# Kernel optimization log

Measured on AMD Instinct MI355X. Metric: run time of the kernel, lower is better.

## Reference

```python
import jax, jax.numpy as jnp
import numpy as np

B, S, D, H = 2, 2048, 768, 12
DK = D // H

def setup_inputs() -> dict:
    key = jax.random.key(0)
    ks = jax.random.split(key, 11)
    sc = 0.02
    inp = {
        'Q': jax.random.normal(ks[0], (B, S, D), jnp.float32),
        'K': jax.random.normal(ks[1], (B, S, D), jnp.float32),
        'V': jax.random.normal(ks[2], (B, S, D), jnp.float32),
        # causal mask, broadcastable over batch and heads (1 = keep, 0 = mask)
        'mask': jnp.tril(jnp.ones((S, S), jnp.int32))[None, None, :, :],
        'Wq': jax.random.normal(ks[3], (D, D), jnp.float32) * sc,
        'bq': jax.random.normal(ks[4], (D,), jnp.float32) * sc,
        'Wk': jax.random.normal(ks[5], (D, D), jnp.float32) * sc,
        'bk': jax.random.normal(ks[6], (D,), jnp.float32) * sc,
        'Wv': jax.random.normal(ks[7], (D, D), jnp.float32) * sc,
        'bv': jax.random.normal(ks[8], (D,), jnp.float32) * sc,
        'Wo': jax.random.normal(ks[9], (D, D), jnp.float32) * sc,
        'bo': jax.random.normal(ks[10], (D,), jnp.float32) * sc,
    }
    return inp

def _split_heads(x):
    # [B,S,D] -> [B,H,S,DK]
    return x.reshape(B, S, H, DK).transpose(0, 2, 1, 3)

def reference(Q, K, V, mask, Wq, bq, Wk, bk, Wv, bv, Wo, bo):
    # torch Linear: y = x @ W.T + b
    q = _split_heads(Q @ Wq.T + bq)
    k = _split_heads(K @ Wk.T + bk)
    v = _split_heads(V @ Wv.T + bv)
    scores = jnp.einsum('bhqd,bhkd->bhqk', q, k) / jnp.sqrt(jnp.float32(DK))
    scores = jnp.where(mask == 0, jnp.float32(-1e9), scores)
    attn = jax.nn.softmax(scores, axis=-1)
    out = jnp.einsum('bhqk,bhkd->bhqd', attn, v)  # [B,H,S,DK]
    out = out.transpose(0, 2, 1, 3).reshape(B, S, D)
    return out @ Wo.T + bo
```

## Files before the change

kernel.cpp:

```cpp
#include <hip/hip_runtime.h>
#include <hip/hip_bf16.h>

#define H_  12
#define S_  2048
#define D_  768
#define DK_ 64

typedef __bf16 bf16x8 __attribute__((ext_vector_type(8)));
typedef __bf16 bf16x4 __attribute__((ext_vector_type(4)));
typedef short  short4v __attribute__((ext_vector_type(4)));
typedef float  f32x4  __attribute__((ext_vector_type(4)));

__device__ inline f32x4 mfma_bf16(bf16x8 a, bf16x8 b, f32x4 c) {
  return __builtin_amdgcn_mfma_f32_16x16x32_bf16(a, b, c, 0, 0, 0);
}

__device__ inline f32x4 mfma16(bf16x4 a, bf16x4 b, f32x4 c) {
#if __has_builtin(__builtin_amdgcn_mfma_f32_16x16x16bf16_1k)
  short4v as = __builtin_bit_cast(short4v, a);
  short4v bs = __builtin_bit_cast(short4v, b);
  return __builtin_amdgcn_mfma_f32_16x16x16bf16_1k(as, bs, c, 0, 0, 0);
#else
  asm("s_nop 1\n\tv_mfma_f32_16x16x16_bf16 %0, %1, %2, %0"
      : "+v"(c) : "v"(a), "v"(b));
  return c;
#endif
}

__device__ inline bf16x8 cvt2bf16(f32x4 a, f32x4 b) {
  bf16x8 r;
  r[0] = (__bf16)a[0]; r[1] = (__bf16)a[1];
  r[2] = (__bf16)a[2]; r[3] = (__bf16)a[3];
  r[4] = (__bf16)b[0]; r[5] = (__bf16)b[1];
  r[6] = (__bf16)b[2]; r[7] = (__bf16)b[3];
  return r;
}

__global__ __launch_bounds__(256, 4)
void qkv_proj(const float* __restrict__ Q, const float* __restrict__ K,
              const float* __restrict__ V,
              const float* __restrict__ Wq, const float* __restrict__ Wk,
              const float* __restrict__ Wv,
              const float* __restrict__ bq, const float* __restrict__ bk,
              const float* __restrict__ bv,
              __hip_bfloat16* __restrict__ q_ws,
              __hip_bfloat16* __restrict__ k_ws,
              __hip_bfloat16* __restrict__ vT_ws)
{
  __shared__ alignas(16) __hip_bfloat16 Ald[2][64][40];
  __shared__ alignas(16) __hip_bfloat16 Bld[2][128][40];

  const int z = blockIdx.z;
  const float* X    = (z == 0) ? Q  : (z == 1) ? K  : V;
  const float* W    = (z == 0) ? Wq : (z == 1) ? Wk : Wv;
  const float* bias = (z == 0) ? bq : (z == 1) ? bk : bv;
  __hip_bfloat16* out = (z == 0) ? q_ws : (z == 1) ? k_ws : vT_ws;
  const bool vmode = (z == 2);
  const float osc = (z == 0) ? 0.125f : 1.0f;

  const int t    = threadIdx.x;
  const int w    = t >> 6;
  const int lane = t & 63;
  const int l15  = lane & 15;
  const int quad = lane >> 4;
  const int m0 = blockIdx.x * 64;
  const int n0 = blockIdx.y * 128;
  const int wm = (w >> 1) * 32;
  const int wn = (w & 1) * 64;

  const f32x4 fzero = {0.f, 0.f, 0.f, 0.f};
  f32x4 acc[2][4];
#pragma unroll
  for (int i = 0; i < 2; ++i)
#pragma unroll
    for (int j = 0; j < 4; ++j) acc[i][j] = fzero;

  const int arow = t >> 2, agr = t & 3;
  const float* Asrc  = X + (size_t)(m0 + arow) * D_ + agr * 8;
  const float* Bsrc0 = W + (size_t)(n0 + arow) * D_ + agr * 8;
  const float* Bsrc1 = W + (size_t)(n0 + arow + 64) * D_ + agr * 8;

  f32x4 a0 = *(const f32x4*)(Asrc), a1 = *(const f32x4*)(Asrc + 4);
  f32x4 b00 = *(const f32x4*)(Bsrc0), b01 = *(const f32x4*)(Bsrc0 + 4);
  f32x4 b10 = *(const f32x4*)(Bsrc1), b11 = *(const f32x4*)(Bsrc1 + 4);
  *(bf16x8*)&Ald[0][arow][agr * 8]      = cvt2bf16(a0, a1);
  *(bf16x8*)&Bld[0][arow][agr * 8]      = cvt2bf16(b00, b01);
  *(bf16x8*)&Bld[0][arow + 64][agr * 8] = cvt2bf16(b10, b11);

  for (int k0 = 0; k0 < D_; k0 += 32) {
    const int p = (k0 >> 5) & 1;
    __syncthreads();
    const int kn = k0 + 32;
    if (kn < D_) {
      a0  = *(const f32x4*)(Asrc + kn);  a1  = *(const f32x4*)(Asrc + kn + 4);
      b00 = *(const f32x4*)(Bsrc0 + kn); b01 = *(const f32x4*)(Bsrc0 + kn + 4);
      b10 = *(const f32x4*)(Bsrc1 + kn); b11 = *(const f32x4*)(Bsrc1 + kn + 4);
    }

    bf16x8 af[2], bfr[4];
#pragma unroll
    for (int i = 0; i < 2; ++i) af[i]  = *(const bf16x8*)&Ald[p][wm + 16 * i + l15][quad * 8];
#pragma unroll
    for (int j = 0; j < 4; ++j) bfr[j] = *(const bf16x8*)&Bld[p][wn + 16 * j + l15][quad * 8];
#pragma unroll
    for (int i = 0; i < 2; ++i)
#pragma unroll
      for (int j = 0; j < 4; ++j)
        acc[i][j] = mfma_bf16(af[i], bfr[j], acc[i][j]);

    if (kn < D_) {
      *(bf16x8*)&Ald[p ^ 1][arow][agr * 8]      = cvt2bf16(a0, a1);
      *(bf16x8*)&Bld[p ^ 1][arow][agr * 8]      = cvt2bf16(b00, b01);
      *(bf16x8*)&Bld[p ^ 1][arow + 64][agr * 8] = cvt2bf16(b10, b11);
    }
  }

#pragma unroll
  for (int j = 0; j < 4; ++j) {
    const int n_g = n0 + wn + 16 * j + l15;
    const float bv = bias[n_g];
    const int hh = n_g >> 6, dk = n_g & (DK_ - 1);
#pragma unroll
    for (int i = 0; i < 2; ++i) {
      const int mbase = m0 + wm + 16 * i + quad * 4;
#pragma unroll
      for (int r = 0; r < 4; ++r) {
        const int m_g = mbase + r;
        const int bb = m_g >> 11, ss = m_g & (S_ - 1);
        const float vout = (acc[i][j][r] + bv) * osc;
        size_t idx;
        if (vmode)
          idx = (((size_t)(bb * H_ + hh)) * DK_ + dk) * S_ + ss;
        else
          idx = (((size_t)(bb * H_ + hh)) * S_ + ss) * DK_ + dk;
        out[idx] = __float2bfloat16(vout);
      }
    }
  }
}

__global__ __launch_bounds__(256, 4)
void o_proj(const __hip_bfloat16* __restrict__ Xb,
            const float* __restrict__ W,
            const float* __restrict__ bias,
            float* __restrict__ outf)
{
  __shared__ alignas(16) __hip_bfloat16 Ald[2][64][40];
  __shared__ alignas(16) __hip_bfloat16 Bld[2][64][40];

  const int t    = threadIdx.x;
  const int w    = t >> 6;
  const int lane = t & 63;
  const int l15  = lane & 15;
  const int quad = lane >> 4;
  const int m0 = blockIdx.x * 64;
  const int n0 = blockIdx.y * 64;
  const int wm = 16 * w;

  const f32x4 fzero = {0.f, 0.f, 0.f, 0.f};
  f32x4 acc[4];
#pragma unroll
  for (int j = 0; j < 4; ++j) acc[j] = fzero;

  const int arow = t >> 2, agr = t & 3;
  const __hip_bfloat16* Asrc = Xb + (size_t)(m0 + arow) * D_ + agr * 8;
  const float* Bsrc = W + (size_t)(n0 + arow) * D_ + agr * 8;

  bf16x8 a_r = *(const bf16x8*)(Asrc);
  f32x4 b0 = *(const f32x4*)(Bsrc), b1 = *(const f32x4*)(Bsrc + 4);
  *(bf16x8*)&Ald[0][arow][agr * 8] = a_r;
  *(bf16x8*)&Bld[0][arow][agr * 8] = cvt2bf16(b0, b1);

  for (int k0 = 0; k0 < D_; k0 += 32) {
    const int p = (k0 >> 5) & 1;
    __syncthreads();
    const int kn = k0 + 32;
    if (kn < D_) {
      a_r = *(const bf16x8*)(Asrc + kn);
      b0 = *(const f32x4*)(Bsrc + kn); b1 = *(const f32x4*)(Bsrc + kn + 4);
    }

    bf16x8 af = *(const bf16x8*)&Ald[p][wm + l15][quad * 8];
    bf16x8 bfr[4];
#pragma unroll
    for (int j = 0; j < 4; ++j) bfr[j] = *(const bf16x8*)&Bld[p][16 * j + l15][quad * 8];
#pragma unroll
    for (int j = 0; j < 4; ++j)
      acc[j] = mfma_bf16(af, bfr[j], acc[j]);

    if (kn < D_) {
      *(bf16x8*)&Ald[p ^ 1][arow][agr * 8] = a_r;
      *(bf16x8*)&Bld[p ^ 1][arow][agr * 8] = cvt2bf16(b0, b1);
    }
  }

#pragma unroll
  for (int j = 0; j < 4; ++j) {
    const int n_g = n0 + 16 * j + l15;
    const float bv = bias[n_g];
    const int mbase = m0 + wm + quad * 4;
#pragma unroll
    for (int r = 0; r < 4; ++r)
      outf[(size_t)(mbase + r) * D_ + n_g] = acc[j][r] + bv;
  }
}

__global__ __launch_bounds__(256, 4)
void flash_attn(const __hip_bfloat16* __restrict__ q_ws,
                const __hip_bfloat16* __restrict__ k_ws,
                const __hip_bfloat16* __restrict__ vT_ws,
                __hip_bfloat16* __restrict__ o_ws)
{
  __shared__ alignas(16) __hip_bfloat16 Kld[128][72];
  __shared__ alignas(16) __hip_bfloat16 Vld[64][136];

  const int t = threadIdx.x, w = t >> 6, lane = t & 63;
  const int l15 = lane & 15, quad = lane >> 4;
  const int bh = blockIdx.y;
  const int b = bh / H_, h = bh % H_;
  const int x = blockIdx.x;
  const int tLo = x, tHi = 63 - x;
  const int myTile = (w < 2) ? tLo : tHi;
  const int qbase = myTile * 32 + 16 * (w & 1);
  const int qg = qbase + l15;
  const int myNkt = (myTile >> 2) + 1;
  const int nktT  = (tHi >> 2) + 1;
  const size_t hbase = (size_t)bh * S_ * DK_;
  const size_t vtb   = (size_t)bh * DK_ * S_;

  bf16x8 qf[2];
#pragma unroll
  for (int kk = 0; kk < 2; ++kk)
    qf[kk] = *(const bf16x8*)(q_ws + hbase + (size_t)qg * DK_ + kk * 32 + quad * 8);

  const f32x4 fzero = {0.f, 0.f, 0.f, 0.f};
  f32x4 accO[4];
#pragma unroll
  for (int jd = 0; jd < 4; ++jd) accO[jd] = fzero;
  float mI = -1.0e30f, lI = 0.f;

  const int tr = t >> 3, kg = t & 7;
  const int tv = t >> 4, vg = t & 15;
  const __hip_bfloat16* Kbase = k_ws + hbase + (size_t)tr * DK_ + kg * 8;
  const __hip_bfloat16* Vbase = vT_ws + vtb + (size_t)tv * S_ + vg * 8;

  bf16x8 rK[4], rV[4];
#pragma unroll
  for (int it = 0; it < 4; ++it) {
    rK[it] = *(const bf16x8*)(Kbase + (size_t)(32 * it) * DK_);
    rV[it] = *(const bf16x8*)(Vbase + (size_t)(16 * it) * S_);
  }

  for (int kt = 0; kt < nktT; ++kt) {
#pragma unroll
    for (int it = 0; it < 4; ++it) {
      *(bf16x8*)&Kld[32 * it + tr][kg * 8] = rK[it];
      *(bf16x8*)&Vld[16 * it + tv][vg * 8] = rV[it];
    }
    __syncthreads();

    if (kt + 1 < nktT) {
      const int k0n = (kt + 1) * 128;
#pragma unroll
      for (int it = 0; it < 4; ++it) {
        rK[it] = *(const bf16x8*)(Kbase + (size_t)(k0n + 32 * it) * DK_);
        rV[it] = *(const bf16x8*)(Vbase + (size_t)(16 * it) * S_ + k0n);
      }
    }

    if (kt < myNkt) {
      const int k0 = kt * 128;
      f32x4 st[8];
#pragma unroll
      for (int j = 0; j < 8; ++j) {
        bf16x8 kf0 = *(const bf16x8*)&Kld[16 * j + l15][quad * 8];
        bf16x8 kf1 = *(const bf16x8*)&Kld[16 * j + l15][32 + quad * 8];
        st[j] = mfma_bf16(kf0, qf[0], fzero);
        st[j] = mfma_bf16(kf1, qf[1], st[j]);
      }

      if (kt == myNkt - 1) {
#pragma unroll
        for (int j = 0; j < 8; ++j)
#pragma unroll
          for (int r = 0; r < 4; ++r) {
            const int kcg = k0 + 16 * j + quad * 4 + r;
            if (kcg > qg) st[j][r] = -1.0e9f;
          }
      }

      float tm = st[0][0];
#pragma unroll
      for (int j = 0; j < 8; ++j)
#pragma unroll
        for (int r = 0; r < 4; ++r) tm = fmaxf(tm, st[j][r]);
      tm = fmaxf(tm, __shfl_xor(tm, 16));
      tm = fmaxf(tm, __shfl_xor(tm, 32));

      const float mnew = fmaxf(mI, tm);
      const float al = __expf(mI - mnew);
      mI = mnew;
      float rs = 0.f;
#pragma unroll
      for (int j = 0; j < 8; ++j)
#pragma unroll
        for (int r = 0; r < 4; ++r) {
          const float pv = __expf(st[j][r] - mnew);
          st[j][r] = pv;
          rs += pv;
        }
      rs += __shfl_xor(rs, 16);
      rs += __shfl_xor(rs, 32);
      lI = lI * al + rs;
#pragma unroll
      for (int jd = 0; jd < 4; ++jd)
#pragma unroll
        for (int r = 0; r < 4; ++r) accO[jd][r] *= al;

      bf16x4 pb[8];
#pragma unroll
      for (int j = 0; j < 8; ++j) {
        pb[j][0] = (__bf16)st[j][0]; pb[j][1] = (__bf16)st[j][1];
        pb[j][2] = (__bf16)st[j][2]; pb[j][3] = (__bf16)st[j][3];
      }

#pragma unroll
      for (int jd = 0; jd < 4; ++jd)
#pragma unroll
        for (int j = 0; j < 8; ++j) {
          bf16x4 vf = *(const bf16x4*)&Vld[16 * jd + l15][16 * j + quad * 4];
          accO[jd] = mfma16(vf, pb[j], accO[jd]);
        }
    }
    __syncthreads();
  }

  const float inv = 1.f / lI;
#pragma unroll
  for (int jd = 0; jd < 4; ++jd) {
    bf16x4 ov;
#pragma unroll
    for (int r = 0; r < 4; ++r) ov[r] = (__bf16)(accO[jd][r] * inv);
    *(bf16x4*)(o_ws + ((size_t)b * S_ + qg) * D_ + h * DK_ + 16 * jd + quad * 4) = ov;
  }
}

extern "C" void kernel_launch(void* const* d_in, const int* in_sizes, int n_in,
                              void* d_out, int out_size, void* d_ws, size_t ws_size,
                              hipStream_t stream) {
  (void)in_sizes; (void)n_in; (void)out_size; (void)ws_size;
  const float* Q  = (const float*)d_in[0];
  const float* K  = (const float*)d_in[1];
  const float* V  = (const float*)d_in[2];
  const float* Wq = (const float*)d_in[4];
  const float* bq = (const float*)d_in[5];
  const float* Wk = (const float*)d_in[6];
  const float* bk = (const float*)d_in[7];
  const float* Wv = (const float*)d_in[8];
  const float* bv = (const float*)d_in[9];
  const float* Wo = (const float*)d_in[10];
  const float* bo = (const float*)d_in[11];
  float* out = (float*)d_out;

  const size_t NEL = (size_t)2 * S_ * D_;
  __hip_bfloat16* q_ws  = (__hip_bfloat16*)d_ws;
  __hip_bfloat16* k_ws  = q_ws  + NEL;
  __hip_bfloat16* vT_ws = k_ws  + NEL;
  __hip_bfloat16* o_ws  = vT_ws + NEL;

  qkv_proj<<<dim3(64, 6, 3), 256, 0, stream>>>(Q, K, V, Wq, Wk, Wv, bq, bk, bv,
                                               q_ws, k_ws, vT_ws);
  flash_attn<<<dim3(32, 24), 256, 0, stream>>>(q_ws, k_ws, vT_ws, o_ws);
  o_proj<<<dim3(64, 12), 256, 0, stream>>>(o_ws, Wo, bo, out);
}
```

Before: 214.1 us.

## Pre-convert weights to bf16, use direct-to-LDS loads, swizzle, larger tiles, exp2 softmax

Adds a kernel that converts all four weight matrices to bf16 once per call. The projection GEMMs then stream the bf16 weights into swizzled, unpadded LDS through global_load_lds, and the tiles grow to 128x128 for QKV and 64x128 for the output projection. The Q scale now includes log2(e), so the attention softmax can use the hardware exp2 instruction. In exchange, double-buffering in LDS is replaced by a single buffer with two barriers per k-step, and the extra conversion kernel adds a launch plus weight traffic.

```diff
diff --git a/kernel.cpp b/kernel.cpp
--- a/kernel.cpp
+++ b/kernel.cpp
@@ -10,6 +10,12 @@
 typedef __bf16 bf16x4 __attribute__((ext_vector_type(4)));
 typedef short  short4v __attribute__((ext_vector_type(4)));
 typedef float  f32x4  __attribute__((ext_vector_type(4)));
+
+#define QSCALE 0.1803368801111137f
+
+__device__ inline float exp2_fast(float x) {
+  return __builtin_amdgcn_exp2f(x);
+}
 
 __device__ inline f32x4 mfma_bf16(bf16x8 a, bf16x8 b, f32x4 c) {
   return __builtin_amdgcn_mfma_f32_16x16x32_bf16(a, b, c, 0, 0, 0);
@@ -27,6 +33,12 @@
 #endif
 }
 
+__device__ inline void gload16(const void* g, void* l) {
+  __builtin_amdgcn_global_load_lds(
+      (const __attribute__((address_space(1))) void*)g,
+      (__attribute__((address_space(3))) void*)l, 16, 0, 0);
+}
+
 __device__ inline bf16x8 cvt2bf16(f32x4 a, f32x4 b) {
   bf16x8 r;
   r[0] = (__bf16)a[0]; r[1] = (__bf16)a[1];
@@ -36,83 +48,107 @@
   return r;
 }
 
-__global__ __launch_bounds__(256, 4)
+__global__ __launch_bounds__(256)
+void conv_w(const float* __restrict__ Wq, const float* __restrict__ Wk,
+            const float* __restrict__ Wv, const float* __restrict__ Wo,
+            __hip_bfloat16* __restrict__ out)
+{
+  const int i8 = blockIdx.x * 256 + threadIdx.x;
+  const int mat = i8 / 73728;
+  const int off = (i8 - mat * 73728) * 8;
+  const float* src = (mat == 0) ? Wq : (mat == 1) ? Wk : (mat == 2) ? Wv : Wo;
+  f32x4 a = *(const f32x4*)(src + off);
+  f32x4 b = *(const f32x4*)(src + off + 4);
+  *(bf16x8*)(out + (size_t)mat * 589824 + off) = cvt2bf16(a, b);
+}
+
+__global__ __launch_bounds__(256, 3)
 void qkv_proj(const float* __restrict__ Q, const float* __restrict__ K,
               const float* __restrict__ V,
-              const float* __restrict__ Wq, const float* __restrict__ Wk,
-              const float* __restrict__ Wv,
+              const __hip_bfloat16* __restrict__ Wb,
               const float* __restrict__ bq, const float* __restrict__ bk,
               const float* __restrict__ bv,
               __hip_bfloat16* __restrict__ q_ws,
               __hip_bfloat16* __restrict__ k_ws,
               __hip_bfloat16* __restrict__ vT_ws)
 {
-  __shared__ alignas(16) __hip_bfloat16 Ald[2][64][40];
-  __shared__ alignas(16) __hip_bfloat16 Bld[2][128][40];
+  __shared__ alignas(16) __hip_bfloat16 Ald[128 * 32];
+  __shared__ alignas(16) __hip_bfloat16 Bld[128 * 32];
 
   const int z = blockIdx.z;
   const float* X    = (z == 0) ? Q  : (z == 1) ? K  : V;
-  const float* W    = (z == 0) ? Wq : (z == 1) ? Wk : Wv;
   const float* bias = (z == 0) ? bq : (z == 1) ? bk : bv;
+  const __hip_bfloat16* Wz = Wb + (size_t)z * 589824;
   __hip_bfloat16* out = (z == 0) ? q_ws : (z == 1) ? k_ws : vT_ws;
   const bool vmode = (z == 2);
-  const float osc = (z == 0) ? 0.125f : 1.0f;
+  const float osc = (z == 0) ? QSCALE : 1.0f;
 
   const int t    = threadIdx.x;
   const int w    = t >> 6;
   const int lane = t & 63;
   const int l15  = lane & 15;
   const int quad = lane >> 4;
-  const int m0 = blockIdx.x * 64;
+  const int m0 = blockIdx.x * 128;
   const int n0 = blockIdx.y * 128;
-  const int wm = (w >> 1) * 32;
+  const int wm = (w >> 1) * 64;
   const int wn = (w & 1) * 64;
 
   const f32x4 fzero = {0.f, 0.f, 0.f, 0.f};
-  f32x4 acc[2][4];
-#pragma unroll
-  for (int i = 0; i < 2; ++i)
+  f32x4 acc[4][4];
+#pragma unroll
+  for (int i = 0; i < 4; ++i)
 #pragma unroll
     for (int j = 0; j < 4; ++j) acc[i][j] = fzero;
 
-  const int arow = t >> 2, agr = t & 3;
-  const float* Asrc  = X + (size_t)(m0 + arow) * D_ + agr * 8;
-  const float* Bsrc0 = W + (size_t)(n0 + arow) * D_ + agr * 8;
-  const float* Bsrc1 = W + (size_t)(n0 + arow + 64) * D_ + agr * 8;
-
-  f32x4 a0 = *(const f32x4*)(Asrc), a1 = *(const f32x4*)(Asrc + 4);
-  f32x4 b00 = *(const f32x4*)(Bsrc0), b01 = *(const f32x4*)(Bsrc0 + 4);
-  f32x4 b10 = *(const f32x4*)(Bsrc1), b11 = *(const f32x4*)(Bsrc1 + 4);
-  *(bf16x8*)&Ald[0][arow][agr * 8]      = cvt2bf16(a0, a1);
-  *(bf16x8*)&Bld[0][arow][agr * 8]      = cvt2bf16(b00, b01);
-  *(bf16x8*)&Bld[0][arow + 64][agr * 8] = cvt2bf16(b10, b11);
+  const int ar = t >> 2, ac = t & 3;
+  const int sw = ac ^ ((ar >> 1) & 3);
+  const float* As0 = X + (size_t)(m0 + ar) * D_ + ac * 8;
+  const float* As1 = X + (size_t)(m0 + ar + 64) * D_ + ac * 8;
+  __hip_bfloat16* Aw0 = &Ald[((ar)      * 4 + sw) * 8];
+  __hip_bfloat16* Aw1 = &Ald[((ar + 64) * 4 + sw) * 8];
+
+  const int bp = (t & 3) ^ (((t >> 2) >> 1) & 3);
+  const __hip_bfloat16* Bs0 = Wz + (size_t)(n0 + (t >> 2)) * D_ + bp * 8;
+  const __hip_bfloat16* Bs1 = Wz + (size_t)(n0 + (t >> 2) + 64) * D_ + bp * 8;
+  __hip_bfloat16* Bd0 = &Bld[t * 8];
+  __hip_bfloat16* Bd1 = &Bld[(t + 256) * 8];
+
+  int agrn[4], bgrn[4];
+#pragma unroll
+  for (int i = 0; i < 4; ++i) {
+    int row = wm + 16 * i + l15;
+    agrn[i] = (row * 4 + (quad ^ ((row >> 1) & 3))) * 8;
+    row = wn + 16 * i + l15;
+    bgrn[i] = (row * 4 + (quad ^ ((row >> 1) & 3))) * 8;
+  }
+
+  f32x4 a00 = *(const f32x4*)As0, a01 = *(const f32x4*)(As0 + 4);
+  f32x4 a10 = *(const f32x4*)As1, a11 = *(const f32x4*)(As1 + 4);
 
   for (int k0 = 0; k0 < D_; k0 += 32) {
-    const int p = (k0 >> 5) & 1;
-    __syncthreads();
+    *(bf16x8*)Aw0 = cvt2bf16(a00, a01);
+    *(bf16x8*)Aw1 = cvt2bf16(a10, a11);
+    gload16(Bs0 + k0, Bd0);
+    gload16(Bs1 + k0, Bd1);
+    __syncthreads();
+
     const int kn = k0 + 32;
     if (kn < D_) {
-      a0  = *(const f32x4*)(Asrc + kn);  a1  = *(const f32x4*)(Asrc + kn + 4);
-      b00 = *(const f32x4*)(Bsrc0 + kn); b01 = *(const f32x4*)(Bsrc0 + kn + 4);
-      b10 = *(const f32x4*)(Bsrc1 + kn); b11 = *(const f32x4*)(Bsrc1 + kn + 4);
-    }
-
-    bf16x8 af[2], bfr[4];
-#pragma unroll
-    for (int i = 0; i < 2; ++i) af[i]  = *(const bf16x8*)&Ald[p][wm + 16 * i + l15][quad * 8];
-#pragma unroll
-    for (int j = 0; j < 4; ++j) bfr[j] = *(const bf16x8*)&Bld[p][wn + 16 * j + l15][quad * 8];
-#pragma unroll
-    for (int i = 0; i < 2; ++i)
+      a00 = *(const f32x4*)(As0 + kn); a01 = *(const f32x4*)(As0 + kn + 4);
+      a10 = *(const f32x4*)(As1 + kn); a11 = *(const f32x4*)(As1 + kn + 4);
+    }
+
+    bf16x8 af[4], bfr[4];
+#pragma unroll
+    for (int i = 0; i < 4; ++i) af[i]  = *(const bf16x8*)&Ald[agrn[i]];
+#pragma unroll
+    for (int j = 0; j < 4; ++j) bfr[j] = *(const bf16x8*)&Bld[bgrn[j]];
+#pragma unroll
+    for (int i = 0; i < 4; ++i)
 #pragma unroll
       for (int j = 0; j < 4; ++j)
         acc[i][j] = mfma_bf16(af[i], bfr[j], acc[i][j]);
-
-    if (kn < D_) {
-      *(bf16x8*)&Ald[p ^ 1][arow][agr * 8]      = cvt2bf16(a0, a1);
-      *(bf16x8*)&Bld[p ^ 1][arow][agr * 8]      = cvt2bf16(b00, b01);
-      *(bf16x8*)&Bld[p ^ 1][arow + 64][agr * 8] = cvt2bf16(b10, b11);
-    }
+    __syncthreads();
   }
 
 #pragma unroll
@@ -121,7 +157,7 @@
     const float bv = bias[n_g];
     const int hh = n_g >> 6, dk = n_g & (DK_ - 1);
 #pragma unroll
-    for (int i = 0; i < 2; ++i) {
+    for (int i = 0; i < 4; ++i) {
       const int mbase = m0 + wm + 16 * i + quad * 4;
 #pragma unroll
       for (int r = 0; r < 4; ++r) {
@@ -141,12 +177,12 @@
 
 __global__ __launch_bounds__(256, 4)
 void o_proj(const __hip_bfloat16* __restrict__ Xb,
-            const float* __restrict__ W,
+            const __hip_bfloat16* __restrict__ Wob,
             const float* __restrict__ bias,
             float* __restrict__ outf)
 {
-  __shared__ alignas(16) __hip_bfloat16 Ald[2][64][40];
-  __shared__ alignas(16) __hip_bfloat16 Bld[2][64][40];
+  __shared__ alignas(16) __hip_bfloat16 Ald[64 * 32];
+  __shared__ alignas(16) __hip_bfloat16 Bld[128 * 32];
 
   const int t    = threadIdx.x;
   const int w    = t >> 6;
@@ -154,54 +190,67 @@
   const int l15  = lane & 15;
   const int quad = lane >> 4;
   const int m0 = blockIdx.x * 64;
-  const int n0 = blockIdx.y * 64;
-  const int wm = 16 * w;
+  const int n0 = blockIdx.y * 128;
+  const int wm = (w >> 1) * 32;
+  const int wn = (w & 1) * 64;
 
   const f32x4 fzero = {0.f, 0.f, 0.f, 0.f};
-  f32x4 acc[4];
-#pragma unroll
-  for (int j = 0; j < 4; ++j) acc[j] = fzero;
-
-  const int arow = t >> 2, agr = t & 3;
-  const __hip_bfloat16* Asrc = Xb + (size_t)(m0 + arow) * D_ + agr * 8;
-  const float* Bsrc = W + (size_t)(n0 + arow) * D_ + agr * 8;
-
-  bf16x8 a_r = *(const bf16x8*)(Asrc);
-  f32x4 b0 = *(const f32x4*)(Bsrc), b1 = *(const f32x4*)(Bsrc + 4);
-  *(bf16x8*)&Ald[0][arow][agr * 8] = a_r;
-  *(bf16x8*)&Bld[0][arow][agr * 8] = cvt2bf16(b0, b1);
+  f32x4 acc[2][4];
+#pragma unroll
+  for (int i = 0; i < 2; ++i)
+#pragma unroll
+    for (int j = 0; j < 4; ++j) acc[i][j] = fzero;
+
+  const int ap = (t & 3) ^ (((t >> 2) >> 1) & 3);
+  const __hip_bfloat16* As  = Xb  + (size_t)(m0 + (t >> 2)) * D_ + ap * 8;
+  const __hip_bfloat16* Bs0 = Wob + (size_t)(n0 + (t >> 2)) * D_ + ap * 8;
+  const __hip_bfloat16* Bs1 = Wob + (size_t)(n0 + (t >> 2) + 64) * D_ + ap * 8;
+  __hip_bfloat16* Ad  = &Ald[t * 8];
+  __hip_bfloat16* Bd0 = &Bld[t * 8];
+  __hip_bfloat16* Bd1 = &Bld[(t + 256) * 8];
+
+  int agrn[2], bgrn[4];
+#pragma unroll
+  for (int i = 0; i < 2; ++i) {
+    const int row = wm + 16 * i + l15;
+    agrn[i] = (row * 4 + (quad ^ ((row >> 1) & 3))) * 8;
+  }
+#pragma unroll
+  for (int j = 0; j < 4; ++j) {
+    const int row = wn + 16 * j + l15;
+    bgrn[j] = (row * 4 + (quad ^ ((row >> 1) & 3))) * 8;
+  }
 
   for (int k0 = 0; k0 < D_; k0 += 32) {
-    const int p = (k0 >> 5) & 1;
-    __syncthreads();
-    const int kn = k0 + 32;
-    if (kn < D_) {
-      a_r = *(const bf16x8*)(Asrc + kn);
-      b0 = *(const f32x4*)(Bsrc + kn); b1 = *(const f32x4*)(Bsrc + kn + 4);
-    }
-
-    bf16x8 af = *(const bf16x8*)&Ald[p][wm + l15][quad * 8];
-    bf16x8 bfr[4];
-#pragma unroll
-    for (int j = 0; j < 4; ++j) bfr[j] = *(const bf16x8*)&Bld[p][16 * j + l15][quad * 8];
-#pragma unroll
-    for (int j = 0; j < 4; ++j)
-      acc[j] = mfma_bf16(af, bfr[j], acc[j]);
-
-    if (kn < D_) {
-      *(bf16x8*)&Ald[p ^ 1][arow][agr * 8] = a_r;
-      *(bf16x8*)&Bld[p ^ 1][arow][agr * 8] = cvt2bf16(b0, b1);
-    }
+    gload16(As + k0, Ad);
+    gload16(Bs0 + k0, Bd0);
+    gload16(Bs1 + k0, Bd1);
+    __syncthreads();
+
+    bf16x8 af[2], bfr[4];
+#pragma unroll
+    for (int i = 0; i < 2; ++i) af[i]  = *(const bf16x8*)&Ald[agrn[i]];
+#pragma unroll
+    for (int j = 0; j < 4; ++j) bfr[j] = *(const bf16x8*)&Bld[bgrn[j]];
+#pragma unroll
+    for (int i = 0; i < 2; ++i)
+#pragma unroll
+      for (int j = 0; j < 4; ++j)
+        acc[i][j] = mfma_bf16(af[i], bfr[j], acc[i][j]);
+    __syncthreads();
   }
 
 #pragma unroll
   for (int j = 0; j < 4; ++j) {
-    const int n_g = n0 + 16 * j + l15;
+    const int n_g = n0 + wn + 16 * j + l15;
     const float bv = bias[n_g];
-    const int mbase = m0 + wm + quad * 4;
-#pragma unroll
-    for (int r = 0; r < 4; ++r)
-      outf[(size_t)(mbase + r) * D_ + n_g] = acc[j][r] + bv;
+#pragma unroll
+    for (int i = 0; i < 2; ++i) {
+      const int mbase = m0 + wm + 16 * i + quad * 4;
+#pragma unroll
+      for (int r = 0; r < 4; ++r)
+        outf[(size_t)(mbase + r) * D_ + n_g] = acc[i][j][r] + bv;
+    }
   }
 }
 
@@ -298,14 +347,14 @@
       tm = fmaxf(tm, __shfl_xor(tm, 32));
 
       const float mnew = fmaxf(mI, tm);
-      const float al = __expf(mI - mnew);
+      const float al = exp2_fast(mI - mnew);
       mI = mnew;
       float rs = 0.f;
 #pragma unroll
       for (int j = 0; j < 8; ++j)
 #pragma unroll
         for (int r = 0; r < 4; ++r) {
-          const float pv = __expf(st[j][r] - mnew);
+          const float pv = exp2_fast(st[j][r] - mnew);
           st[j][r] = pv;
           rs += pv;
         }
@@ -362,14 +411,17 @@
   const float* bo = (const float*)d_in[11];
   float* out = (float*)d_out;
 
+  const size_t WEL = (size_t)4 * 589824;
   const size_t NEL = (size_t)2 * S_ * D_;
-  __hip_bfloat16* q_ws  = (__hip_bfloat16*)d_ws;
+  __hip_bfloat16* wb    = (__hip_bfloat16*)d_ws;
+  __hip_bfloat16* q_ws  = wb + WEL;
   __hip_bfloat16* k_ws  = q_ws  + NEL;
   __hip_bfloat16* vT_ws = k_ws  + NEL;
   __hip_bfloat16* o_ws  = vT_ws + NEL;
 
-  qkv_proj<<<dim3(64, 6, 3), 256, 0, stream>>>(Q, K, V, Wq, Wk, Wv, bq, bk, bv,
+  conv_w<<<1152, 256, 0, stream>>>(Wq, Wk, Wv, Wo, wb);
+  qkv_proj<<<dim3(32, 6, 3), 256, 0, stream>>>(Q, K, V, wb, bq, bk, bv,
                                                q_ws, k_ws, vT_ws);
   flash_attn<<<dim3(32, 24), 256, 0, stream>>>(q_ws, k_ws, vT_ws, o_ws);
-  o_proj<<<dim3(64, 12), 256, 0, stream>>>(o_ws, Wo, bo, out);
-}
+  o_proj<<<dim3(64, 6), 256, 0, stream>>>(o_ws, wb + (size_t)3 * 589824, bo, out);
+}
```

Measured after the change: 207.3 us. 3.2% less time.
